# Kernel optimization log

Measured on AMD Instinct MI355X. Metric: run time of the kernel, lower is better.

## Reference

```python
import jax, jax.numpy as jnp
import numpy as np

N, K, D_IN, D_H, D_A, N_CLS = 8192, 10, 1024, 512, 256, 4


def setup_inputs() -> dict:
    key = jax.random.key(0)
    ks = jax.random.split(key, 20)
    def lin(k, fan_in, shape):
        return jax.random.normal(k, shape, dtype=jnp.float32) / np.sqrt(fan_in)
    return {
        "x_path": jax.random.normal(ks[0], (N, D_IN), dtype=jnp.float32),
        "cluster_id": jax.random.randint(ks[1], (N,), 0, K),
        # per-cluster phi MLP (Linear 1024->512, ReLU, Linear 512->512, ReLU); dropout = eval identity
        "W1": lin(ks[2], D_IN, (K, D_IN, D_H)), "b1": jnp.zeros((K, D_H), jnp.float32),
        "W2": lin(ks[3], D_H, (K, D_H, D_H)), "b2": jnp.zeros((K, D_H), jnp.float32),
        # attention_net fc: Linear 512->512 + ReLU
        "fc_W": lin(ks[4], D_H, (D_H, D_H)), "fc_b": jnp.zeros((D_H,), jnp.float32),
        # Attn_Net_Gated: a=tanh(Va), b=sigmoid(Vb), A=(a*b)@Vc
        "Va": lin(ks[5], D_H, (D_H, D_A)), "ba": jnp.zeros((D_A,), jnp.float32),
        "Vb": lin(ks[6], D_H, (D_H, D_A)), "bb": jnp.zeros((D_A,), jnp.float32),
        "Vc": lin(ks[7], D_A, (D_A, 1)), "bc": jnp.zeros((1,), jnp.float32),
        # rho: Linear 512->256 + ReLU
        "rho_W": lin(ks[8], D_H, (D_H, D_A)), "rho_b": jnp.zeros((D_A,), jnp.float32),
        # classifier: Linear 256->4
        "cls_W": lin(ks[9], D_A, (D_A, N_CLS)), "cls_b": jnp.zeros((N_CLS,), jnp.float32),
    }


def reference(x_path, cluster_id, W1, b1, W2, b2, fc_W, fc_b,
              Va, ba, Vb, bb, Vc, bc, rho_W, rho_b, cls_W, cls_b):
    # mask[k, n] = 1 if patch n belongs to cluster k
    mask = (cluster_id[None, :] == jnp.arange(K)[:, None]).astype(x_path.dtype)  # [K, N]

    # per-cluster 2-layer MLP applied to all patches, masked mean-pool (= AdaptiveAvgPool1d(1))
    def phi(W1i, b1i, W2i, b2i):
        h = jax.nn.relu(x_path @ W1i + b1i)          # [N, 512]
        return jax.nn.relu(h @ W2i + b2i)            # [N, 512]
    y = jax.vmap(phi)(W1, b1, W2, b2)                # [K, N, 512]
    cnt = mask.sum(axis=1)                           # [K]
    pooled = jnp.einsum('kn,knd->kd', mask, y) / jnp.maximum(cnt, 1.0)[:, None]  # [K, 512]
    # empty cluster -> zeros (matches torch.zeros((1,512)) branch since b terms are zero via where)
    pooled = jnp.where(cnt[:, None] > 0, pooled, 0.0)

    # attention_net: fc + gated attention
    h = jax.nn.relu(pooled @ fc_W + fc_b)            # [K, 512]
    a = jnp.tanh(h @ Va + ba)                        # [K, 256]
    b = jax.nn.sigmoid(h @ Vb + bb)                  # [K, 256]
    A = (a * b) @ Vc + bc                            # [K, 1]
    A = jax.nn.softmax(A.T, axis=1)                  # [1, K]
    h_path = A @ h                                   # [1, 512]
    h_path = jax.nn.relu(h_path @ rho_W + rho_b)[0]  # [256]
    logits = (h_path @ cls_W + cls_b)[None, :]       # [1, 4]
    Y_hat = jnp.argmax(logits, axis=1, keepdims=True)
    hazards = jax.nn.sigmoid(logits)
    S = jnp.cumprod(1.0 - hazards, axis=1)
    return hazards, S, Y_hat
```

## Files before the change

### kernel.cpp

```cpp
#include <hip/hip_runtime.h>
#include <math.h>

#define NPATCH 8192
#define KC     10
#define DIN    1024
#define DH     512
#define DA     256
#define NCLS   4

#define TM  32
#define LDA 520

typedef unsigned short u16;
typedef short bf16x8 __attribute__((ext_vector_type(8)));
typedef float f32x4  __attribute__((ext_vector_type(4)));

#define OFF_CNT   0
#define OFF_BAR   48
#define OFF_IDX   64
#define OFF_PSUM  327744
#define OFF_H     348224
#define OFF_H2    368768
#define OFF_SRED  369792
#define OFF_W1P   373888
#define OFF_W2P   10859648

__device__ __forceinline__ u16 f2bf(float f) {
  union { float f; unsigned u; } v; v.f = f;
  unsigned r = (v.u + 0x7fffu + ((v.u >> 16) & 1u)) >> 16;
  return (u16)r;
}

__device__ __forceinline__ unsigned cvtpk(float lo, float hi) {
  unsigned r;
  asm("v_cvt_pk_bf16_f32 %0, %1, %2" : "=v"(r) : "v"(lo), "v"(hi));
  return r;
}

struct __align__(8) U16x4 { u16 x, y, z, w; };
union BF8U { bf16x8 v; unsigned u[4]; };

#define W1_TILES (KC * (DIN / 32) * (DH / 32))
#define W2_TILES (KC * (DH / 32) * (DH / 32))
#define NB_BUCKET 32
#define NB_PREP (NB_BUCKET + W1_TILES + W2_TILES)

__global__ __launch_bounds__(256) void prep_kernel(
    const int* __restrict__ cid, int* __restrict__ cnt,
    int* __restrict__ idxlist, const float* __restrict__ W1,
    const float* __restrict__ W2, u16* __restrict__ W1p,
    u16* __restrict__ W2p, float* __restrict__ psum) {
  int b = blockIdx.x, t = threadIdx.x;
  if (b < NB_BUCKET) {
    int g = b * 256 + t;
    if (g < KC * DH) psum[g] = 0.f;
    __shared__ int lcnt[KC], lbase[KC];
    if (t < KC) lcnt[t] = 0;
    __syncthreads();
    int n = b * 256 + t;
    int k = cid[n];
    int myoff = atomicAdd(&lcnt[k], 1);
    __syncthreads();
    if (t < KC) lbase[t] = atomicAdd(&cnt[t], lcnt[t]);
    __syncthreads();
    idxlist[k * NPATCH + lbase[k] + myoff] = n;
  } else {
    __shared__ u16 tile[32][33];
    int bb = b - NB_BUCKET;
    const float* src;
    u16* dst;
    if (bb < W1_TILES) {
      int k = bb / 512, rem = bb % 512;
      int kb = rem / 16, n0 = (rem % 16) * 32;
      src = W1 + (size_t)k * DIN * DH + (size_t)kb * 32 * DH + n0;
      dst = W1p + (((size_t)(k * 32 + kb) * 512 + n0) * 32);
    } else {
      int b2 = bb - W1_TILES;
      int k = b2 / 256, rem = b2 % 256;
      int kb = rem / 16, n0 = (rem % 16) * 32;
      src = W2 + (size_t)k * DH * DH + (size_t)kb * 32 * DH + n0;
      dst = W2p + (((size_t)(k * 16 + kb) * 512 + n0) * 32);
    }
    {
      int ki = t >> 3, n4 = (t & 7) * 4;
      float4 v = *(const float4*)&src[(size_t)ki * DH + n4];
      tile[ki][n4 + 0] = f2bf(v.x);
      tile[ki][n4 + 1] = f2bf(v.y);
      tile[ki][n4 + 2] = f2bf(v.z);
      tile[ki][n4 + 3] = f2bf(v.w);
    }
    __syncthreads();
    {
      int n = t >> 3, ki = (t & 7) * 4;
      U16x4 o = {tile[ki + 0][n], tile[ki + 1][n], tile[ki + 2][n],
                 tile[ki + 3][n]};
      *(U16x4*)&dst[(size_t)n * 32 + ki] = o;
    }
  }
}

__global__ __launch_bounds__(512, 4) void phi_kernel(
    const float* __restrict__ x, const u16* __restrict__ W1p,
    const u16* __restrict__ W2p, const float* __restrict__ b1,
    const float* __restrict__ b2, const int* __restrict__ cnt,
    const int* __restrict__ idxlist, float* __restrict__ psum) {
  __shared__ __align__(16) u16 A0[TM * LDA];
  __shared__ __align__(16) u16 A1[TM * LDA];
  __shared__ int ridx[TM];

  const int tid = threadIdx.x;
  const int w = tid >> 6, lane = tid & 63;
  const int quad = lane >> 4, l16 = lane & 15;

  int cn[KC];
#pragma unroll
  for (int i = 0; i < KC; ++i) cn[i] = cnt[i];
  int G = 0;
#pragma unroll
  for (int i = 0; i < KC; ++i) G += (cn[i] + TM - 1) >> 5;

  const int s = blockIdx.x & 7, j = blockIdx.x >> 3;
  const int lo = (G * s) >> 3, hi = (G * (s + 1)) >> 3;

  for (int g = lo + j; g < hi; g += 64) {
    int kk = 0, rg = g, cntk = cn[0];
#pragma unroll
    for (int i = 0; i < KC - 1; ++i) {
      int nch = (cn[i] + TM - 1) >> 5;
      if (rg >= nch) { kk = i + 1; rg -= nch; cntk = cn[i + 1]; }
    }
    const int base = rg * TM;

    if (tid < TM)
      ridx[tid] = (base + tid < cntk) ? idxlist[kk * NPATCH + base + tid] : -1;
    __syncthreads();

#pragma unroll
    for (int u8 = 0; u8 < 8; ++u8) {
      const int kh = u8 & 1;
      const int r = w * 4 + (u8 >> 1);
      int src = ridx[r];
      BF8U o;
      if (src >= 0) {
        const float4* xp =
            (const float4*)(x + (size_t)src * DIN + kh * 512 + lane * 8);
        float4 v0 = xp[0], v1 = xp[1];
        o.u[0] = cvtpk(v0.x, v0.y);
        o.u[1] = cvtpk(v0.z, v0.w);
        o.u[2] = cvtpk(v1.x, v1.y);
        o.u[3] = cvtpk(v1.z, v1.w);
      } else {
        o.u[0] = 0; o.u[1] = 0; o.u[2] = 0; o.u[3] = 0;
      }
      u16* dstbuf = kh ? A1 : A0;
      *(bf16x8*)&dstbuf[r * LDA + lane * 8] = o.v;
    }
    __syncthreads();

    const f32x4 zero4 = {0.f, 0.f, 0.f, 0.f};
    f32x4 acc[2][4];
#pragma unroll
    for (int m = 0; m < 2; ++m)
#pragma unroll
      for (int nt = 0; nt < 4; ++nt) acc[m][nt] = zero4;

#pragma unroll
    for (int kh = 0; kh < 2; ++kh) {
      const u16* Abuf = kh ? A1 : A0;
      const u16* wb = W1p + ((size_t)(kk * 32 + kh * 16) * 512 +
                             (w * 64 + l16)) * 32 + quad * 8;
      bf16x8 B[2][4];
#pragma unroll
      for (int nt = 0; nt < 4; ++nt)
        B[0][nt] = *(const bf16x8*)(wb + nt * 512);
#pragma unroll
      for (int ks = 0; ks < 16; ++ks) {
        const int cur = ks & 1, nxt = cur ^ 1;
        if (ks < 15) {
#pragma unroll
          for (int nt = 0; nt < 4; ++nt)
            B[nxt][nt] =
                *(const bf16x8*)(wb + (size_t)(ks + 1) * 16384 + nt * 512);
        }
        bf16x8 af0 = *(const bf16x8*)&Abuf[l16 * LDA + ks * 32 + quad * 8];
        bf16x8 af1 =
            *(const bf16x8*)&Abuf[(16 + l16) * LDA + ks * 32 + quad * 8];
#pragma unroll
        for (int nt = 0; nt < 4; ++nt) {
          acc[0][nt] = __builtin_amdgcn_mfma_f32_16x16x32_bf16(
              af0, B[cur][nt], acc[0][nt], 0, 0, 0);
          acc[1][nt] = __builtin_amdgcn_mfma_f32_16x16x32_bf16(
              af1, B[cur][nt], acc[1][nt], 0, 0, 0);
        }
      }
    }
    __syncthreads();

#pragma unroll
    for (int m = 0; m < 2; ++m)
#pragma unroll
      for (int nt = 0; nt < 4; ++nt) {
        int c = w * 64 + nt * 16 + l16;
        float bias = b1[kk * DH + c];
#pragma unroll
        for (int r = 0; r < 4; ++r) {
          int row = m * 16 + quad * 4 + r;
          A0[row * LDA + c] = f2bf(fmaxf(acc[m][nt][r] + bias, 0.f));
        }
      }
    __syncthreads();

    f32x4 acc2[2][4];
#pragma unroll
    for (int m = 0; m < 2; ++m)
#pragma unroll
      for (int nt = 0; nt < 4; ++nt) acc2[m][nt] = zero4;

    {
      const u16* wb2 = W2p + ((size_t)(kk * 16) * 512 +
                              (w * 64 + l16)) * 32 + quad * 8;
      bf16x8 B[2][4];
#pragma unroll
      for (int nt = 0; nt < 4; ++nt)
        B[0][nt] = *(const bf16x8*)(wb2 + nt * 512);
#pragma unroll
      for (int ks = 0; ks < 16; ++ks) {
        const int cur = ks & 1, nxt = cur ^ 1;
        if (ks < 15) {
#pragma unroll
          for (int nt = 0; nt < 4; ++nt)
            B[nxt][nt] =
                *(const bf16x8*)(wb2 + (size_t)(ks + 1) * 16384 + nt * 512);
        }
        bf16x8 af0 = *(const bf16x8*)&A0[l16 * LDA + ks * 32 + quad * 8];
        bf16x8 af1 =
            *(const bf16x8*)&A0[(16 + l16) * LDA + ks * 32 + quad * 8];
#pragma unroll
        for (int nt = 0; nt < 4; ++nt) {
          acc2[0][nt] = __builtin_amdgcn_mfma_f32_16x16x32_bf16(
              af0, B[cur][nt], acc2[0][nt], 0, 0, 0);
          acc2[1][nt] = __builtin_amdgcn_mfma_f32_16x16x32_bf16(
              af1, B[cur][nt], acc2[1][nt], 0, 0, 0);
        }
      }
    }

    float vmask[2][4];
#pragma unroll
    for (int m = 0; m < 2; ++m)
#pragma unroll
      for (int r = 0; r < 4; ++r)
        vmask[m][r] = (base + m * 16 + quad * 4 + r < cntk) ? 1.f : 0.f;

#pragma unroll
    for (int nt = 0; nt < 4; ++nt) {
      int col = w * 64 + nt * 16 + l16;
      float bias = b2[kk * DH + col];
      float sv = 0.f;
#pragma unroll
      for (int m = 0; m < 2; ++m)
#pragma unroll
        for (int r = 0; r < 4; ++r)
          sv += vmask[m][r] * fmaxf(acc2[m][nt][r] + bias, 0.f);
      sv += __shfl_xor(sv, 16, 64);
      sv += __shfl_xor(sv, 32, 64);
      if (quad == 0) atomicAdd(&psum[kk * DH + col], sv);
    }
  }
}

#define NTB 64

__device__ __forceinline__ void bar_arrive_wait(int* bar) {
  __syncthreads();
  if (threadIdx.x == 0) {
    __threadfence();
    __hip_atomic_fetch_add(bar, 1, __ATOMIC_RELEASE, __HIP_MEMORY_SCOPE_AGENT);
    while (__hip_atomic_load(bar, __ATOMIC_ACQUIRE,
                             __HIP_MEMORY_SCOPE_AGENT) < NTB) {
      __builtin_amdgcn_s_sleep(1);
    }
  }
  __syncthreads();
}

__global__ __launch_bounds__(256) void tail_kernel(
    const float* __restrict__ psum, const int* __restrict__ cnt,
    const float* __restrict__ fcW, const float* __restrict__ fcb,
    const float* __restrict__ Va, const float* __restrict__ ba,
    const float* __restrict__ Vb, const float* __restrict__ bb_,
    const float* __restrict__ Vc, const float* __restrict__ rhoW,
    const float* __restrict__ rhob, const float* __restrict__ clsW,
    const float* __restrict__ clsb, float* __restrict__ hstore,
    float* __restrict__ sred, float* __restrict__ h2g,
    int* __restrict__ bar, float* __restrict__ out) {
  __shared__ float p_sh[KC * DH];
  __shared__ float r1[2560];
  __shared__ float r2[2560];
  __shared__ float invs[KC];
  __shared__ float gate_sh[4 * KC];
  __shared__ float ws_sh[KC];
  __shared__ float hp_sh[DH];
  const int tid = threadIdx.x;
  const int b = blockIdx.x;

  if (tid < KC) {
    int c = cnt[tid];
    invs[tid] = (c > 0) ? 1.f / (float)c : 0.f;
  }
  __syncthreads();
#pragma unroll
  for (int it = 0; it < KC * DH / 256; ++it) {
    int e = it * 256 + tid;
    p_sh[e] = psum[e] * invs[e >> 9];
  }
  __syncthreads();
  {
    const int jj = tid & 7, dq = tid >> 3;
    const int j0 = b * 8;
    float acc[KC];
#pragma unroll
    for (int k = 0; k < KC; ++k) acc[k] = 0.f;
#pragma unroll 4
    for (int i = 0; i < 16; ++i) {
      int d = dq * 16 + i;
      float wv = fcW[(size_t)d * DH + j0 + jj];
#pragma unroll
      for (int k = 0; k < KC; ++k) acc[k] = fmaf(p_sh[k * DH + d], wv, acc[k]);
    }
#pragma unroll
    for (int k = 0; k < KC; ++k) r1[(dq * 8 + jj) * KC + k] = acc[k];
    __syncthreads();
    if (tid < 8 * KC) {
      int jj2 = tid / KC, k = tid % KC;
      float s = 0.f;
#pragma unroll
      for (int q = 0; q < 32; ++q) s += r1[(q * 8 + jj2) * KC + k];
      hstore[k * DH + j0 + jj2] = fmaxf(s + fcb[j0 + jj2], 0.f);
    }
  }
  bar_arrive_wait(&bar[0]);

#pragma unroll
  for (int it = 0; it < KC * DH / 256; ++it) {
    int e = it * 256 + tid;
    p_sh[e] = hstore[e];
  }
  __syncthreads();
  {
    const int jj = tid & 3, dq = tid >> 2;
    const int j0 = b * 4;
    float sa[KC], sb[KC];
#pragma unroll
    for (int k = 0; k < KC; ++k) { sa[k] = 0.f; sb[k] = 0.f; }
#pragma unroll 4
    for (int i = 0; i < 8; ++i) {
      int d = dq * 8 + i;
      float va = Va[(size_t)d * DA + j0 + jj];
      float vb = Vb[(size_t)d * DA + j0 + jj];
#pragma unroll
      for (int k = 0; k < KC; ++k) {
        float h = p_sh[k * DH + d];
        sa[k] = fmaf(h, va, sa[k]);
        sb[k] = fmaf(h, vb, sb[k]);
      }
    }
#pragma unroll
    for (int k = 0; k < KC; ++k) {
      r1[(dq * 4 + jj) * KC + k] = sa[k];
      r2[(dq * 4 + jj) * KC + k] = sb[k];
    }
    __syncthreads();
    if (tid < 4 * KC) {
      int jj2 = tid / KC, k = tid % KC;
      float ta = 0.f, tb = 0.f;
#pragma unroll
      for (int q = 0; q < 64; ++q) {
        ta += r1[(q * 4 + jj2) * KC + k];
        tb += r2[(q * 4 + jj2) * KC + k];
      }
      float a = tanhf(ta + ba[j0 + jj2]);
      float g = 1.f / (1.f + expf(-(tb + bb_[j0 + jj2])));
      gate_sh[jj2 * KC + k] = a * g * Vc[j0 + jj2];
    }
    __syncthreads();
    if (tid < KC) {
      float s = 0.f;
#pragma unroll
      for (int jj2 = 0; jj2 < 4; ++jj2) s += gate_sh[jj2 * KC + tid];
      sred[b * 16 + tid] = s;
    }
  }
  bar_arrive_wait(&bar[1]);

  if (tid < KC) {
    float s = 0.f;
    for (int q = 0; q < NTB; ++q) s += sred[q * 16 + tid];
    ws_sh[tid] = s;
  }
  __syncthreads();
  if (tid == 0) {
    float m = -1e30f;
#pragma unroll
    for (int k2 = 0; k2 < KC; ++k2) m = fmaxf(m, ws_sh[k2]);
    float Z = 0.f;
#pragma unroll
    for (int k2 = 0; k2 < KC; ++k2) {
      float e = expf(ws_sh[k2] - m);
      ws_sh[k2] = e;
      Z += e;
    }
    float iZ = 1.f / Z;
#pragma unroll
    for (int k2 = 0; k2 < KC; ++k2) ws_sh[k2] *= iZ;
  }
  __syncthreads();
#pragma unroll
  for (int it = 0; it < 2; ++it) {
    int d = it * 256 + tid;
    float s = 0.f;
#pragma unroll
    for (int k2 = 0; k2 < KC; ++k2) s = fmaf(ws_sh[k2], p_sh[k2 * DH + d], s);
    hp_sh[d] = s;
  }
  __syncthreads();
  {
    const int jj = tid & 3, dq = tid >> 2;
    const int j0 = b * 4;
    float acc = 0.f;
#pragma unroll 4
    for (int i = 0; i < 8; ++i) {
      int d = dq * 8 + i;
      acc = fmaf(hp_sh[d], rhoW[(size_t)d * DA + j0 + jj], acc);
    }
    r1[dq * 4 + jj] = acc;
    __syncthreads();
    if (tid < 4) {
      float s = 0.f;
#pragma unroll
      for (int q = 0; q < 64; ++q) s += r1[q * 4 + tid];
      h2g[j0 + tid] = fmaxf(s + rhob[j0 + tid], 0.f);
    }
  }

  if (b != 0) {
    __syncthreads();
    if (tid == 0) {
      __threadfence();
      __hip_atomic_fetch_add(&bar[2], 1, __ATOMIC_RELEASE,
                             __HIP_MEMORY_SCOPE_AGENT);
    }
    return;
  }
  bar_arrive_wait(&bar[2]);
  {
    float h = h2g[tid];
#pragma unroll
    for (int c = 0; c < NCLS; ++c)
      r1[c * 256 + tid] = h * clsW[(size_t)tid * NCLS + c];
    __syncthreads();
    for (int s = 128; s > 0; s >>= 1) {
      if (tid < s) {
#pragma unroll
      for (int c = 0; c < NCLS; ++c)
          r1[c * 256 + tid] += r1[c * 256 + tid + s];
      }
      __syncthreads();
    }
    if (tid == 0) {
      float lg[NCLS], hz[NCLS];
      int best = 0;
#pragma unroll
      for (int c = 0; c < NCLS; ++c) {
        lg[c] = r1[c * 256] + clsb[c];
        hz[c] = 1.f / (1.f + expf(-lg[c]));
        if (lg[c] > lg[best]) best = c;
      }
      float S = 1.f;
#pragma unroll
      for (int c = 0; c < NCLS; ++c) out[c] = hz[c];
#pragma unroll
      for (int c = 0; c < NCLS; ++c) {
        S *= (1.f - hz[c]);
        out[NCLS + c] = S;
      }
      out[2 * NCLS] = (float)best;
    }
  }
}

extern "C" void kernel_launch(void* const* d_in, const int* in_sizes, int n_in,
                              void* d_out, int out_size, void* d_ws,
                              size_t ws_size, hipStream_t stream) {
  const float* x    = (const float*)d_in[0];
  const int*   cid  = (const int*)d_in[1];
  const float* W1   = (const float*)d_in[2];
  const float* b1   = (const float*)d_in[3];
  const float* W2   = (const float*)d_in[4];
  const float* b2   = (const float*)d_in[5];
  const float* fcW  = (const float*)d_in[6];
  const float* fcb  = (const float*)d_in[7];
  const float* Va   = (const float*)d_in[8];
  const float* ba   = (const float*)d_in[9];
  const float* Vb   = (const float*)d_in[10];
  const float* bb_  = (const float*)d_in[11];
  const float* Vc   = (const float*)d_in[12];
  const float* rhoW = (const float*)d_in[14];
  const float* rhob = (const float*)d_in[15];
  const float* clsW = (const float*)d_in[16];
  const float* clsb = (const float*)d_in[17];
  float* out = (float*)d_out;

  char* ws = (char*)d_ws;
  int*   cnt     = (int*)(ws + OFF_CNT);
  int*   bar     = (int*)(ws + OFF_BAR);
  int*   idxlist = (int*)(ws + OFF_IDX);
  float* psum    = (float*)(ws + OFF_PSUM);
  float* hstore  = (float*)(ws + OFF_H);
  float* h2g     = (float*)(ws + OFF_H2);
  float* sred    = (float*)(ws + OFF_SRED);
  u16*   W1p     = (u16*)(ws + OFF_W1P);
  u16*   W2p     = (u16*)(ws + OFF_W2P);

  (void)hipMemsetAsync(cnt, 0, 64, stream);
  prep_kernel<<<NB_PREP, 256, 0, stream>>>(cid, cnt, idxlist, W1, W2, W1p, W2p,
                                           psum);
  phi_kernel<<<512, 512, 0, stream>>>(x, W1p, W2p, b1, b2, cnt, idxlist, psum);
  tail_kernel<<<NTB, 256, 0, stream>>>(psum, cnt, fcW, fcb, Va, ba, Vb, bb_,
                                       Vc, rhoW, rhob, clsW, clsb, hstore,
                                       sred, h2g, bar, out);
}
```

Before: 204.2 us.

## Deepen weight prefetch to three stages and batch prep tiles per block

The phi kernel's B-operand weight loads now use a three-deep register ring instead of two-deep double buffering. The first W1 fragments are issued before the x gather/convert and the first W2 fragments before the layer-1 epilogue, so global weight latency overlaps other work. The prep kernel handles four weight-transpose tiles per block, cutting the block count by four. This raises register pressure in a kernel launched with 512 threads and min 4 blocks, which could cause spills or lower occupancy.

```diff
diff --git a/kernel.cpp b/kernel.cpp
--- a/kernel.cpp
+++ b/kernel.cpp
@@ -43,7 +43,8 @@
 #define W1_TILES (KC * (DIN / 32) * (DH / 32))
 #define W2_TILES (KC * (DH / 32) * (DH / 32))
 #define NB_BUCKET 32
-#define NB_PREP (NB_BUCKET + W1_TILES + W2_TILES)
+#define WT_PER_BLK 4
+#define NB_PREP (NB_BUCKET + (W1_TILES + W2_TILES) / WT_PER_BLK)
 
 __global__ __launch_bounds__(256) void prep_kernel(
     const int* __restrict__ cid, int* __restrict__ cnt,
@@ -66,35 +67,39 @@
     idxlist[k * NPATCH + lbase[k] + myoff] = n;
   } else {
     __shared__ u16 tile[32][33];
-    int bb = b - NB_BUCKET;
-    const float* src;
-    u16* dst;
-    if (bb < W1_TILES) {
-      int k = bb / 512, rem = bb % 512;
-      int kb = rem / 16, n0 = (rem % 16) * 32;
-      src = W1 + (size_t)k * DIN * DH + (size_t)kb * 32 * DH + n0;
-      dst = W1p + (((size_t)(k * 32 + kb) * 512 + n0) * 32);
-    } else {
-      int b2 = bb - W1_TILES;
-      int k = b2 / 256, rem = b2 % 256;
-      int kb = rem / 16, n0 = (rem % 16) * 32;
-      src = W2 + (size_t)k * DH * DH + (size_t)kb * 32 * DH + n0;
-      dst = W2p + (((size_t)(k * 16 + kb) * 512 + n0) * 32);
-    }
-    {
-      int ki = t >> 3, n4 = (t & 7) * 4;
-      float4 v = *(const float4*)&src[(size_t)ki * DH + n4];
-      tile[ki][n4 + 0] = f2bf(v.x);
-      tile[ki][n4 + 1] = f2bf(v.y);
-      tile[ki][n4 + 2] = f2bf(v.z);
-      tile[ki][n4 + 3] = f2bf(v.w);
-    }
-    __syncthreads();
-    {
-      int n = t >> 3, ki = (t & 7) * 4;
-      U16x4 o = {tile[ki + 0][n], tile[ki + 1][n], tile[ki + 2][n],
-                 tile[ki + 3][n]};
-      *(U16x4*)&dst[(size_t)n * 32 + ki] = o;
+#pragma unroll
+    for (int it = 0; it < WT_PER_BLK; ++it) {
+      int bb = (b - NB_BUCKET) * WT_PER_BLK + it;
+      const float* src;
+      u16* dst;
+      if (bb < W1_TILES) {
+        int k = bb / 512, rem = bb % 512;
+        int kb = rem / 16, n0 = (rem % 16) * 32;
+        src = W1 + (size_t)k * DIN * DH + (size_t)kb * 32 * DH + n0;
+        dst = W1p + (((size_t)(k * 32 + kb) * 512 + n0) * 32);
+      } else {
+        int b2 = bb - W1_TILES;
+        int k = b2 / 256, rem = b2 % 256;
+        int kb = rem / 16, n0 = (rem % 16) * 32;
+        src = W2 + (size_t)k * DH * DH + (size_t)kb * 32 * DH + n0;
+        dst = W2p + (((size_t)(k * 16 + kb) * 512 + n0) * 32);
+      }
+      {
+        int ki = t >> 3, n4 = (t & 7) * 4;
+        float4 v = *(const float4*)&src[(size_t)ki * DH + n4];
+        tile[ki][n4 + 0] = f2bf(v.x);
+        tile[ki][n4 + 1] = f2bf(v.y);
+        tile[ki][n4 + 2] = f2bf(v.z);
+        tile[ki][n4 + 3] = f2bf(v.w);
+      }
+      __syncthreads();
+      {
+        int n = t >> 3, ki = (t & 7) * 4;
+        U16x4 o = {tile[ki + 0][n], tile[ki + 1][n], tile[ki + 2][n],
+                   tile[ki + 3][n]};
+        *(U16x4*)&dst[(size_t)n * 32 + ki] = o;
+      }
+      __syncthreads();
     }
   }
 }
@@ -134,6 +139,15 @@
     if (tid < TM)
       ridx[tid] = (base + tid < cntk) ? idxlist[kk * NPATCH + base + tid] : -1;
     __syncthreads();
+
+    const u16* wb = W1p + ((size_t)(kk * 32) * 512 + (w * 64 + l16)) * 32 +
+                    quad * 8;
+    bf16x8 B[3][4];
+#pragma unroll
+    for (int p = 0; p < 3; ++p)
+#pragma unroll
+      for (int nt = 0; nt < 4; ++nt)
+        B[p][nt] = *(const bf16x8*)(wb + (size_t)p * 16384 + nt * 512);
 
 #pragma unroll
     for (int u8 = 0; u8 < 8; ++u8) {
@@ -165,35 +179,35 @@
       for (int nt = 0; nt < 4; ++nt) acc[m][nt] = zero4;
 
 #pragma unroll
-    for (int kh = 0; kh < 2; ++kh) {
-      const u16* Abuf = kh ? A1 : A0;
-      const u16* wb = W1p + ((size_t)(kk * 32 + kh * 16) * 512 +
-                             (w * 64 + l16)) * 32 + quad * 8;
-      bf16x8 B[2][4];
+    for (int ks = 0; ks < 32; ++ks) {
+      const int cur = ks % 3;
+      const u16* Abuf = (ks < 16) ? A0 : A1;
+      const int ao = (ks & 15) * 32 + quad * 8;
+      bf16x8 af0 = *(const bf16x8*)&Abuf[l16 * LDA + ao];
+      bf16x8 af1 = *(const bf16x8*)&Abuf[(16 + l16) * LDA + ao];
+#pragma unroll
+      for (int nt = 0; nt < 4; ++nt) {
+        acc[0][nt] = __builtin_amdgcn_mfma_f32_16x16x32_bf16(
+            af0, B[cur][nt], acc[0][nt], 0, 0, 0);
+        acc[1][nt] = __builtin_amdgcn_mfma_f32_16x16x32_bf16(
+            af1, B[cur][nt], acc[1][nt], 0, 0, 0);
+      }
+      if (ks < 29) {
+#pragma unroll
+        for (int nt = 0; nt < 4; ++nt)
+          B[cur][nt] =
+              *(const bf16x8*)(wb + (size_t)(ks + 3) * 16384 + nt * 512);
+      }
+    }
+
+    const u16* wb2 = W2p + ((size_t)(kk * 16) * 512 + (w * 64 + l16)) * 32 +
+                     quad * 8;
+#pragma unroll
+    for (int p = 0; p < 3; ++p)
 #pragma unroll
       for (int nt = 0; nt < 4; ++nt)
-        B[0][nt] = *(const bf16x8*)(wb + nt * 512);
-#pragma unroll
-      for (int ks = 0; ks < 16; ++ks) {
-        const int cur = ks & 1, nxt = cur ^ 1;
-        if (ks < 15) {
-#pragma unroll
-          for (int nt = 0; nt < 4; ++nt)
-            B[nxt][nt] =
-                *(const bf16x8*)(wb + (size_t)(ks + 1) * 16384 + nt * 512);
-        }
-        bf16x8 af0 = *(const bf16x8*)&Abuf[l16 * LDA + ks * 32 + quad * 8];
-        bf16x8 af1 =
-            *(const bf16x8*)&Abuf[(16 + l16) * LDA + ks * 32 + quad * 8];
-#pragma unroll
-        for (int nt = 0; nt < 4; ++nt) {
-          acc[0][nt] = __builtin_amdgcn_mfma_f32_16x16x32_bf16(
-              af0, B[cur][nt], acc[0][nt], 0, 0, 0);
-          acc[1][nt] = __builtin_amdgcn_mfma_f32_16x16x32_bf16(
-              af1, B[cur][nt], acc[1][nt], 0, 0, 0);
-        }
-      }
-    }
+        B[p][nt] = *(const bf16x8*)(wb2 + (size_t)p * 16384 + nt * 512);
+
     __syncthreads();
 
 #pragma unroll
@@ -216,32 +230,24 @@
 #pragma unroll
       for (int nt = 0; nt < 4; ++nt) acc2[m][nt] = zero4;
 
-    {
-      const u16* wb2 = W2p + ((size_t)(kk * 16) * 512 +
-                              (w * 64 + l16)) * 32 + quad * 8;
-      bf16x8 B[2][4];
-#pragma unroll
-      for (int nt = 0; nt < 4; ++nt)
-        B[0][nt] = *(const bf16x8*)(wb2 + nt * 512);
-#pragma unroll
-      for (int ks = 0; ks < 16; ++ks) {
-        const int cur = ks & 1, nxt = cur ^ 1;
-        if (ks < 15) {
-#pragma unroll
-          for (int nt = 0; nt < 4; ++nt)
-            B[nxt][nt] =
-                *(const bf16x8*)(wb2 + (size_t)(ks + 1) * 16384 + nt * 512);
-        }
-        bf16x8 af0 = *(const bf16x8*)&A0[l16 * LDA + ks * 32 + quad * 8];
-        bf16x8 af1 =
-            *(const bf16x8*)&A0[(16 + l16) * LDA + ks * 32 + quad * 8];
-#pragma unroll
-        for (int nt = 0; nt < 4; ++nt) {
-          acc2[0][nt] = __builtin_amdgcn_mfma_f32_16x16x32_bf16(
-              af0, B[cur][nt], acc2[0][nt], 0, 0, 0);
-          acc2[1][nt] = __builtin_amdgcn_mfma_f32_16x16x32_bf16(
-              af1, B[cur][nt], acc2[1][nt], 0, 0, 0);
-        }
+#pragma unroll
+    for (int ks = 0; ks < 16; ++ks) {
+      const int cur = ks % 3;
+      const int ao = ks * 32 + quad * 8;
+      bf16x8 af0 = *(const bf16x8*)&A0[l16 * LDA + ao];
+      bf16x8 af1 = *(const bf16x8*)&A0[(16 + l16) * LDA + ao];
+#pragma unroll
+      for (int nt = 0; nt < 4; ++nt) {
+        acc2[0][nt] = __builtin_amdgcn_mfma_f32_16x16x32_bf16(
+            af0, B[cur][nt], acc2[0][nt], 0, 0, 0);
+        acc2[1][nt] = __builtin_amdgcn_mfma_f32_16x16x32_bf16(
+            af1, B[cur][nt], acc2[1][nt], 0, 0, 0);
+      }
+      if (ks < 13) {
+#pragma unroll
+        for (int nt = 0; nt < 4; ++nt)
+          B[cur][nt] =
+              *(const bf16x8*)(wb2 + (size_t)(ks + 3) * 16384 + nt * 512);
       }
     }
 
@@ -462,7 +468,7 @@
     for (int s = 128; s > 0; s >>= 1) {
       if (tid < s) {
 #pragma unroll
-      for (int c = 0; c < NCLS; ++c)
+        for (int c = 0; c < NCLS; ++c)
           r1[c * 256 + tid] += r1[c * 256 + tid + s];
       }
       __syncthreads();
```

After: 205.9 us. About the same (+0.8%).
